# Kernel optimization log

Measured on AMD Instinct MI355X. Metric: run time of the kernel, lower is better.

## Reference

```python
import jax, jax.numpy as jnp
import numpy as np
import math

B, L, S, T = 16, 128, 128, 128
QDIM, FDIM, HID, ODIM = 512, 512, 512, 512

def setup_inputs() -> dict:
    key = jax.random.key(0)
    ks = jax.random.split(key, 9)
    sc = 0.02
    return {
        "query": jax.random.normal(ks[0], (B, L, QDIM), dtype=jnp.float32),
        "src": jax.random.normal(ks[1], (B, S, FDIM), dtype=jnp.float32),
        "trg": jax.random.normal(ks[2], (B, T, FDIM), dtype=jnp.float32),
        "Wq": jax.random.normal(ks[3], (QDIM, HID), dtype=jnp.float32) * sc,
        "bq": jnp.zeros((HID,), dtype=jnp.float32),
        "Ws": jax.random.normal(ks[4], (FDIM, HID), dtype=jnp.float32) * sc,
        "bs": jnp.zeros((HID,), dtype=jnp.float32),
        "Wo": jax.random.normal(ks[5], (FDIM * 2 + QDIM, ODIM), dtype=jnp.float32) * sc,
        "bo": jnp.zeros((ODIM,), dtype=jnp.float32),
    }

def reference(query, src, trg, Wq, bq, Ws, bs, Wo, bo):
    b, l, _ = query.shape
    s = src.shape[1]
    t = trg.shape[1]
    q = query @ Wq + bq            # [b,l,h]
    s_key = src @ Ws + bs          # [b,s,h]  (src_linear == trg_linear, shared weights)
    t_key = trg @ Ws + bs          # [b,t,h]
    # trilinear scores: [b,l,s,t]
    weight = jnp.einsum('blk,bsk,btk->blst', q, s_key, t_key) / math.sqrt(HID)
    weight = jax.nn.softmax(weight.reshape(b, l, s * t), axis=-1).reshape(b, l, s, t)
    s_ctx = jnp.einsum('blst,bsf->blf', weight, src)
    t_ctx = jnp.einsum('blst,btf->blf', weight, trg)
    x = jnp.concatenate((query, s_ctx, t_ctx), axis=-1)
    return x @ Wo + bo
```

## Files before the change

kernel.cpp:

```cpp
#include <hip/hip_runtime.h>
#include <hip/hip_bf16.h>

typedef __attribute__((ext_vector_type(8))) short short8;
typedef __attribute__((ext_vector_type(4))) short short4v;
typedef __attribute__((ext_vector_type(4))) float f32x4;
typedef __attribute__((ext_vector_type(8))) _Float16 half8;

#define DEVINL static __device__ __forceinline__

constexpr float SCORE_SCALE = 0.063758977414048896f;

typedef const __attribute__((address_space(1))) void gv_t;
typedef __attribute__((address_space(3))) void lv_t;
DEVINL void gload16(const void* g, void* l) {
  __builtin_amdgcn_global_load_lds((gv_t*)g, (lv_t*)l, 16, 0, 0);
}

#define SWZ_ADD(v, pat)                                                    \
  v += __int_as_float(__builtin_amdgcn_ds_swizzle(__float_as_int(v), pat))

template <int M, int N>
DEVINL void gemm16(const _Float16* A, const _Float16* B, int K, int lda, int ldb,
                   _Float16* ldsA, _Float16* ldsB, f32x4 acc[M / 32][N / 32])
{
  const int tid = threadIdx.x, lane = tid & 63;
  const int wr = (tid >> 7) & 1, wc = (tid >> 6) & 1;
  constexpr int MA = M / 32, NB = N / 32;
  int aoff[MA], boff[NB];
#pragma unroll
  for (int i = 0; i < MA; ++i) {
    const int ci = tid + i * 256, row = ci >> 3, c = ci & 7;
    aoff[i] = row * lda + ((c ^ (row & 7)) << 3);
  }
#pragma unroll
  for (int i = 0; i < NB; ++i) {
    const int ci = tid + i * 256, row = ci >> 3, c = ci & 7;
    boff[i] = row * ldb + ((c ^ (row & 7)) << 3);
  }
#define G16STAGE(cur, kk)                                                        \
  {                                                                              \
    _Pragma("unroll")                                                            \
    for (int i = 0; i < MA; ++i)                                                 \
      gload16(A + aoff[i] + (kk), ldsA + (cur) * (M * 64) + (tid + i * 256) * 8);\
    _Pragma("unroll")                                                            \
    for (int i = 0; i < NB; ++i)                                                 \
      gload16(B + boff[i] + (kk), ldsB + (cur) * (N * 64) + (tid + i * 256) * 8);\
  }
  G16STAGE(0, 0);
  __syncthreads();
  for (int kk = 0; kk < K; kk += 64) {
    const int cur = (kk >> 6) & 1;
    if (kk + 64 < K) G16STAGE(cur ^ 1, kk + 64);
    const _Float16* bA = ldsA + cur * (M * 64);
    const _Float16* bB = ldsB + cur * (N * 64);
#pragma unroll
    for (int s = 0; s < 2; ++s) {
      const int cg2 = s * 4 + (lane >> 4);
      half8 afr[MA], bfr[NB];
#pragma unroll
      for (int mi = 0; mi < MA; ++mi) {
        const int r = wr * (M / 2) + mi * 16 + (lane & 15);
        afr[mi] = *(const half8*)(bA + r * 64 + ((cg2 ^ (r & 7)) << 3));
      }
#pragma unroll
      for (int ni = 0; ni < NB; ++ni) {
        const int r = wc * (N / 2) + ni * 16 + (lane & 15);
        bfr[ni] = *(const half8*)(bB + r * 64 + ((cg2 ^ (r & 7)) << 3));
      }
#pragma unroll
      for (int mi = 0; mi < MA; ++mi)
#pragma unroll
        for (int ni = 0; ni < NB; ++ni)
          acc[mi][ni] = __builtin_amdgcn_mfma_f32_16x16x32_f16(afr[mi], bfr[ni], acc[mi][ni], 0, 0, 0);
    }
    __syncthreads();
  }
#undef G16STAGE
}

__global__ __launch_bounds__(256) void k_prep(
    const float* __restrict__ query, const float* __restrict__ src,
    const float* __restrict__ trg,
    const float* __restrict__ Wq, const float* __restrict__ Ws,
    const float* __restrict__ Wo,
    _Float16* __restrict__ x, _Float16* __restrict__ srch,
    _Float16* __restrict__ trgh,
    _Float16* __restrict__ WqT, _Float16* __restrict__ WsT,
    _Float16* __restrict__ WoT,
    _Float16* __restrict__ srcT, _Float16* __restrict__ trgT)
{
  __shared__ float t[32][33];
  const int id = blockIdx.x, tid = threadIdx.x;
  if (id < 1536) {
    const int z = id >> 9;
    const int idx8 = (((id & 511) << 8) + tid) * 8;
    const float* in = (z == 0) ? query : (z == 1) ? src : trg;
    float4 va = *(const float4*)(in + idx8);
    float4 vb = *(const float4*)(in + idx8 + 4);
    half8 h;
    h[0] = (_Float16)va.x; h[1] = (_Float16)va.y;
    h[2] = (_Float16)va.z; h[3] = (_Float16)va.w;
    h[4] = (_Float16)vb.x; h[5] = (_Float16)vb.y;
    h[6] = (_Float16)vb.z; h[7] = (_Float16)vb.w;
    if (z == 0) {
      const int row = idx8 >> 9, col = idx8 & 511;
      *(half8*)(x + (size_t)row * 1536 + col) = h;
    } else {
      _Float16* o = (z == 1) ? srch : trgh;
      *(half8*)(o + idx8) = h;
    }
    return;
  }
  const float* in; _Float16* out; int KK, NN, bx, by; size_t bo = 0;
  if (id < 1792)      { const int u = id - 1536; in = Wq;  out = WqT;  KK = 512;  NN = 512; bx = u & 15; by = u >> 4; }
  else if (id < 2048) { const int u = id - 1792; in = Ws;  out = WsT;  KK = 512;  NN = 512; bx = u & 15; by = u >> 4; }
  else if (id < 2816) { const int u = id - 2048; in = Wo;  out = WoT;  KK = 1536; NN = 512; bx = u & 15; by = u >> 4; }
  else if (id < 3840) { const int u = id - 2816; in = src; out = srcT; KK = 128;  NN = 512; bx = u & 15; by = (u >> 4) & 3; bo = (size_t)(u >> 6) * 65536; }
  else                { const int u = id - 3840; in = trg; out = trgT; KK = 128;  NN = 512; bx = u & 15; by = (u >> 4) & 3; bo = (size_t)(u >> 6) * 65536; }
  const int tx = tid & 31, ty = tid >> 5;
  const int k0 = by * 32, n0 = bx * 32;
#pragma unroll
  for (int i = 0; i < 4; ++i)
    t[ty + i * 8][tx] = in[bo + (size_t)(k0 + ty + i * 8) * NN + n0 + tx];
  __syncthreads();
#pragma unroll
  for (int i = 0; i < 4; ++i)
    out[bo + (size_t)(n0 + ty + i * 8) * KK + k0 + tx] = (_Float16)t[tx][ty + i * 8];
}

__global__ __launch_bounds__(256) void k_proj(
    const _Float16* __restrict__ xq, const _Float16* __restrict__ srch,
    const _Float16* __restrict__ trgh,
    const _Float16* __restrict__ WqT, const _Float16* __restrict__ WsT,
    const float* __restrict__ bq, const float* __restrict__ bs,
    _Float16* __restrict__ qh, _Float16* __restrict__ skh,
    _Float16* __restrict__ tkh)
{
  __shared__ __align__(16) _Float16 lds[24576];
  const int z = blockIdx.z;
  const _Float16* A = (z == 0) ? xq : (z == 1) ? srch : trgh;
  const int lda = (z == 0) ? 1536 : 512;
  const _Float16* BT = (z == 0) ? WqT : WsT;
  const float* bias = (z == 0) ? bq : bs;
  const int brow = blockIdx.y * 64, bcol = blockIdx.x * 128;

  f32x4 acc[2][4] = {};
  gemm16<64, 128>(A + (size_t)brow * lda, BT + (size_t)bcol * 512, 512, lda, 512,
                  lds, lds + 8192, acc);

  const int tid = threadIdx.x, lane = tid & 63;
  const int wr = (tid >> 7) & 1, wc = (tid >> 6) & 1;
  const int r0 = wr * 32 + ((lane >> 4) << 2);
  const int c0 = wc * 64 + (lane & 15);
#pragma unroll
  for (int mi = 0; mi < 2; ++mi)
#pragma unroll
    for (int ni = 0; ni < 4; ++ni) {
      const int col = bcol + c0 + ni * 16;
      const float bv = bias[col];
#pragma unroll
      for (int r = 0; r < 4; ++r) {
        const int row = brow + r0 + mi * 16 + r;
        const float v = acc[mi][ni][r] + bv;
        if (z == 0)      qh[(size_t)row * 512 + col] = (_Float16)(v * SCORE_SCALE);
        else if (z == 1) skh[(size_t)row * 512 + col] = (_Float16)v;
        else             tkh[(size_t)row * 512 + col] = (_Float16)v;
      }
    }
}

__global__ __launch_bounds__(512, 4) void k_score(
    const _Float16* __restrict__ qh, const _Float16* __restrict__ skh,
    const _Float16* __restrict__ tkh,
    _Float16* __restrict__ wct)
{
  __shared__ __align__(16) char pool[51200];
  _Float16* qlds = (_Float16*)(pool + 49152);
  float* wsp   = (float*)(pool);
  float* wtp   = (float*)(pool + 4096);
  float* wfin  = (float*)(pool + 8192);
  float* denom = (float*)(pool + 12288);

  const int raw = blockIdx.x;
  const int swz = (raw & 7) * 128 + (raw >> 3);
  const int b = swz >> 6, l0 = (swz & 63) * 2;

  const int tid = threadIdx.x, lane = tid & 63, wid = tid >> 6;
  const int l = wid >> 2, qs = (wid >> 1) & 1, qt = wid & 1;
  const int cg = lane >> 4;
  const int ln = lane & 15;
  const _Float16* skb = skh + (size_t)b * 65536;
  const _Float16* tkb = tkh + (size_t)b * 65536;

  int soff;
  {
    const int row = tid >> 2, c = tid & 3;
    soff = row * 512 + ((c ^ ((row >> 1) & 3)) << 3);
  }

  if (tid < 256) {
    const int li = tid >> 7, e = (tid & 127) * 4;
    *(short4v*)(qlds + li * 512 + e) =
        *(const short4v*)(qh + (size_t)(b * 128 + l0 + li) * 512 + e);
  }

  const int rbase_s = (qs * 64 + ln) * 64;
  const int rbase_t = (qt * 64 + ln) * 64;
  const int sw = (cg ^ ((ln >> 1) & 3)) << 4;

#define KSTAGE(dstbuf, kt)                                                  \
  {                                                                         \
    gload16(skb + soff + (kt) * 32, (dstbuf) + tid * 16);                   \
    gload16(tkb + soff + (kt) * 32, (dstbuf) + 8192 + tid * 16);            \
  }

  f32x4 acc[4][4] = {};
  char* bufA = pool;
  char* bufB = pool + 16384;
  char* bufC = pool + 32768;
  KSTAGE(bufA, 0);
  KSTAGE(bufB, 1);
  asm volatile("s_waitcnt vmcnt(0) lgkmcnt(0)" ::: "memory");
  __builtin_amdgcn_sched_barrier(0);
  __builtin_amdgcn_s_barrier();
  __builtin_amdgcn_sched_barrier(0);

  for (int it = 0; it < 16; ++it) {
    if (it < 14) KSTAGE(bufC, it + 2);
    half8 qv = *(const half8*)(qlds + l * 512 + it * 32 + cg * 8);
    half8 sfr[4], tfr[4];
#pragma unroll
    for (int mi = 0; mi < 4; ++mi)
      sfr[mi] = *(const half8*)(bufA + rbase_s + mi * 1024 + sw);
#pragma unroll
    for (int ni = 0; ni < 4; ++ni)
      tfr[ni] = *(const half8*)(bufA + 8192 + rbase_t + ni * 1024 + sw);
    __builtin_amdgcn_s_setprio(1);
#pragma unroll
    for (int mi = 0; mi < 4; ++mi) {
      half8 a = sfr[mi] * qv;
#pragma unroll
      for (int ni = 0; ni < 4; ++ni)
        acc[mi][ni] = __builtin_amdgcn_mfma_f32_16x16x32_f16(a, tfr[ni], acc[mi][ni], 0, 0, 0);
    }
    __builtin_amdgcn_s_setprio(0);
    if (it < 14) { asm volatile("s_waitcnt vmcnt(2)" ::: "memory"); }
    else         { asm volatile("s_waitcnt vmcnt(0)" ::: "memory"); }
    __builtin_amdgcn_sched_barrier(0);
    __builtin_amdgcn_s_barrier();
    __builtin_amdgcn_sched_barrier(0);
    char* t_ = bufA; bufA = bufB; bufB = bufC; bufC = t_;
  }
#undef KSTAGE

#pragma unroll
  for (int mi = 0; mi < 4; ++mi)
#pragma unroll
    for (int ni = 0; ni < 4; ++ni)
#pragma unroll
      for (int r = 0; r < 4; ++r)
        acc[mi][ni][r] = exp2f(acc[mi][ni][r]);

#pragma unroll
  for (int mi = 0; mi < 4; ++mi)
#pragma unroll
    for (int r = 0; r < 4; ++r) {
      float v = acc[mi][0][r] + acc[mi][1][r] + acc[mi][2][r] + acc[mi][3][r];
      SWZ_ADD(v, 0x041F);
      SWZ_ADD(v, 0x081F);
      SWZ_ADD(v, 0x101F);
      SWZ_ADD(v, 0x201F);
      if ((lane & 15) == 0)
        wsp[(l * 2 + qt) * 128 + qs * 64 + mi * 16 + (lane >> 4) * 4 + r] = v;
    }
#pragma unroll
  for (int ni = 0; ni < 4; ++ni) {
    float v = 0.f;
#pragma unroll
    for (int mi = 0; mi < 4; ++mi)
#pragma unroll
      for (int r = 0; r < 4; ++r) v += acc[mi][ni][r];
    SWZ_ADD(v, 0x401F);
    v += __shfl_xor(v, 32);
    if (lane < 16) wtp[(l * 2 + qs) * 128 + qt * 64 + ni * 16 + lane] = v;
  }
  __syncthreads();

  if (tid < 256) {
    const int li = tid >> 7, idx = tid & 127;
    wfin[(li * 2 + 0) * 128 + idx] =
        wsp[(li * 2 + 0) * 128 + idx] + wsp[(li * 2 + 1) * 128 + idx];
  } else {
    const int u = tid - 256, li = u >> 7, idx = u & 127;
    wfin[(li * 2 + 1) * 128 + idx] =
        wtp[(li * 2 + 0) * 128 + idx] + wtp[(li * 2 + 1) * 128 + idx];
  }
  __syncthreads();
  if (wid < 2) {
    float v = wfin[wid * 256 + lane] + wfin[wid * 256 + lane + 64];
#pragma unroll
    for (int off = 32; off >= 1; off >>= 1) v += __shfl_xor(v, off);
    if (lane == 0) denom[wid] = v;
  }
  __syncthreads();
  const float inv0 = 1.0f / denom[0], inv1 = 1.0f / denom[1];

  if (tid < 256) {
    const int li = tid >> 7, idx = tid & 127;
    const float inv = li ? inv1 : inv0;
    wct[((size_t)(b * 2 + 0) * 128 + l0 + li) * 128 + idx] =
        (_Float16)(wfin[li * 256 + idx] * inv);
  } else {
    const int u = tid - 256, li = u >> 7, idx = u & 127;
    const float inv = li ? inv1 : inv0;
    wct[((size_t)(b * 2 + 1) * 128 + l0 + li) * 128 + idx] =
        (_Float16)(wfin[li * 256 + 128 + idx] * inv);
  }
}

__global__ __launch_bounds__(256) void k_ctx(const _Float16* __restrict__ wct,
                                             const _Float16* __restrict__ srcT,
                                             const _Float16* __restrict__ trgT,
                                             _Float16* __restrict__ x)
{
  __shared__ __align__(16) _Float16 lds[24576];
  const int side = blockIdx.x, fcol = blockIdx.y >> 1, mrow = blockIdx.y & 1;
  const int b = blockIdx.z;
  const _Float16* A  = wct + (size_t)(b * 2 + side) * 16384 + mrow * 64 * 128;
  const _Float16* BT = (side ? trgT : srcT) + (size_t)b * 65536 + fcol * 16384;

  f32x4 acc[2][4] = {};
  gemm16<64, 128>(A, BT, 128, 128, 128, lds, lds + 8192, acc);

  const int tid = threadIdx.x, lane = tid & 63;
  const int wr = (tid >> 7) & 1, wc = (tid >> 6) & 1;
  const int r0 = wr * 32 + ((lane >> 4) << 2);
  const int c0 = wc * 64 + (lane & 15);
  const int xoff = 512 + side * 512 + fcol * 128;
#pragma unroll
  for (int mi = 0; mi < 2; ++mi)
#pragma unroll
    for (int ni = 0; ni < 4; ++ni) {
      const int col = c0 + ni * 16;
#pragma unroll
      for (int r = 0; r < 4; ++r) {
        const int row = mrow * 64 + r0 + mi * 16 + r;
        x[(size_t)(b * 128 + row) * 1536 + xoff + col] = (_Float16)acc[mi][ni][r];
      }
    }
}

__global__ __launch_bounds__(256) void k_out(const _Float16* __restrict__ x,
                                             const _Float16* __restrict__ WoT,
                                             const float* __restrict__ bo,
                                             float* __restrict__ out)
{
  __shared__ __align__(16) _Float16 lds[16384];
  const int brow = blockIdx.y * 64, bcol = blockIdx.x * 64;
  f32x4 acc[2][2] = {};
  gemm16<64, 64>(x + (size_t)brow * 1536, WoT + (size_t)bcol * 1536, 1536, 1536, 1536,
                 lds, lds + 8192, acc);
  const int tid = threadIdx.x, lane = tid & 63;
  const int wr = (tid >> 7) & 1, wc = (tid >> 6) & 1;
  const int r0 = wr * 32 + ((lane >> 4) << 2);
  const int c0 = wc * 32 + (lane & 15);
#pragma unroll
  for (int mi = 0; mi < 2; ++mi)
#pragma unroll
    for (int ni = 0; ni < 2; ++ni) {
      const int col = bcol + c0 + ni * 16;
      const float bv = bo[col];
#pragma unroll
      for (int r = 0; r < 4; ++r) {
        const int row = brow + r0 + mi * 16 + r;
        out[(size_t)row * 512 + col] = acc[mi][ni][r] + bv;
      }
    }
}

extern "C" void kernel_launch(void* const* d_in, const int* in_sizes, int n_in,
                              void* d_out, int out_size, void* d_ws, size_t ws_size,
                              hipStream_t stream)
{
  (void)in_sizes; (void)n_in; (void)out_size; (void)ws_size;
  const float* query = (const float*)d_in[0];
  const float* src   = (const float*)d_in[1];
  const float* trg   = (const float*)d_in[2];
  const float* Wq    = (const float*)d_in[3];
  const float* bq    = (const float*)d_in[4];
  const float* Ws    = (const float*)d_in[5];
  const float* bs    = (const float*)d_in[6];
  const float* Wo    = (const float*)d_in[7];
  const float* bo    = (const float*)d_in[8];
  float* out = (float*)d_out;

  char* w = (char*)d_ws;
  _Float16* x    = (_Float16*)(w);
  _Float16* qh   = (_Float16*)(w + (6u  << 20));
  _Float16* skh  = (_Float16*)(w + (8u  << 20));
  _Float16* tkh  = (_Float16*)(w + (10u << 20));
  _Float16* srch = (_Float16*)(w + (12u << 20));
  _Float16* trgh = (_Float16*)(w + (14u << 20));
  _Float16* WqT  = (_Float16*)(w + (16u << 20));
  _Float16* WsT  = (_Float16*)(w + (16u << 20) + 512 * 512 * 2);
  _Float16* WoT  = (_Float16*)(w + (17u << 20));
  _Float16* srcT = (_Float16*)(w + (19u << 20));
  _Float16* trgT = (_Float16*)(w + (21u << 20));
  _Float16* wct  = (_Float16*)(w + (23u << 20));

  k_prep<<<4864, 256, 0, stream>>>(query, src, trg, Wq, Ws, Wo,
                                   x, srch, trgh, WqT, WsT, WoT, srcT, trgT);
  k_proj<<<dim3(4, 32, 3), 256, 0, stream>>>(x, srch, trgh, WqT, WsT, bq, bs, qh, skh, tkh);
  k_score<<<1024, 512, 0, stream>>>(qh, skh, tkh, wct);
  k_ctx<<<dim3(2, 8, 16), 256, 0, stream>>>(wct, srcT, trgT, x);
  k_out<<<dim3(8, 32), 256, 0, stream>>>(x, WoT, bo, out);
}
```

Measured before the change: 79.52 us.

## Halve k_score block size, each wave computes both query rows

```diff
diff --git a/kernel.cpp b/kernel.cpp
--- a/kernel.cpp
+++ b/kernel.cpp
@@ -169,7 +169,7 @@
     }
 }
 
-__global__ __launch_bounds__(512, 4) void k_score(
+__global__ __launch_bounds__(256, 2) void k_score(
     const _Float16* __restrict__ qh, const _Float16* __restrict__ skh,
     const _Float16* __restrict__ tkh,
     _Float16* __restrict__ wct)
@@ -186,19 +186,21 @@
   const int b = swz >> 6, l0 = (swz & 63) * 2;
 
   const int tid = threadIdx.x, lane = tid & 63, wid = tid >> 6;
-  const int l = wid >> 2, qs = (wid >> 1) & 1, qt = wid & 1;
+  const int qs = wid >> 1, qt = wid & 1;
   const int cg = lane >> 4;
   const int ln = lane & 15;
   const _Float16* skb = skh + (size_t)b * 65536;
   const _Float16* tkb = tkh + (size_t)b * 65536;
 
-  int soff;
+  int soff[2];
+#pragma unroll
+  for (int j = 0; j < 2; ++j) {
+    const int ci = j * 256 + tid;
+    const int row = ci >> 2, c = ci & 3;
+    soff[j] = row * 512 + ((c ^ ((row >> 1) & 3)) << 3);
+  }
+
   {
-    const int row = tid >> 2, c = tid & 3;
-    soff = row * 512 + ((c ^ ((row >> 1) & 3)) << 3);
-  }
-
-  if (tid < 256) {
     const int li = tid >> 7, e = (tid & 127) * 4;
     *(short4v*)(qlds + li * 512 + e) =
         *(const short4v*)(qh + (size_t)(b * 128 + l0 + li) * 512 + e);
@@ -210,11 +212,14 @@
 
 #define KSTAGE(dstbuf, kt)                                                  \
   {                                                                         \
-    gload16(skb + soff + (kt) * 32, (dstbuf) + tid * 16);                   \
-    gload16(tkb + soff + (kt) * 32, (dstbuf) + 8192 + tid * 16);            \
-  }
-
-  f32x4 acc[4][4] = {};
+    _Pragma("unroll")                                                       \
+    for (int j = 0; j < 2; ++j) {                                           \
+      gload16(skb + soff[j] + (kt) * 32, (dstbuf) + (j * 256 + tid) * 16);  \
+      gload16(tkb + soff[j] + (kt) * 32, (dstbuf) + 8192 + (j * 256 + tid) * 16); \
+    }                                                                       \
+  }
+
+  f32x4 acc[2][4][4] = {};
   char* bufA = pool;
   char* bufB = pool + 16384;
   char* bufC = pool + 32768;
@@ -227,7 +232,8 @@
 
   for (int it = 0; it < 16; ++it) {
     if (it < 14) KSTAGE(bufC, it + 2);
-    half8 qv = *(const half8*)(qlds + l * 512 + it * 32 + cg * 8);
+    half8 qv0 = *(const half8*)(qlds + it * 32 + cg * 8);
+    half8 qv1 = *(const half8*)(qlds + 512 + it * 32 + cg * 8);
     half8 sfr[4], tfr[4];
 #pragma unroll
     for (int mi = 0; mi < 4; ++mi)
@@ -238,13 +244,16 @@
     __builtin_amdgcn_s_setprio(1);
 #pragma unroll
     for (int mi = 0; mi < 4; ++mi) {
-      half8 a = sfr[mi] * qv;
-#pragma unroll
-      for (int ni = 0; ni < 4; ++ni)
-        acc[mi][ni] = __builtin_amdgcn_mfma_f32_16x16x32_f16(a, tfr[ni], acc[mi][ni], 0, 0, 0);
+      half8 a0 = sfr[mi] * qv0;
+      half8 a1 = sfr[mi] * qv1;
+#pragma unroll
+      for (int ni = 0; ni < 4; ++ni) {
+        acc[0][mi][ni] = __builtin_amdgcn_mfma_f32_16x16x32_f16(a0, tfr[ni], acc[0][mi][ni], 0, 0, 0);
+        acc[1][mi][ni] = __builtin_amdgcn_mfma_f32_16x16x32_f16(a1, tfr[ni], acc[1][mi][ni], 0, 0, 0);
+      }
     }
     __builtin_amdgcn_s_setprio(0);
-    if (it < 14) { asm volatile("s_waitcnt vmcnt(2)" ::: "memory"); }
+    if (it < 14) { asm volatile("s_waitcnt vmcnt(4)" ::: "memory"); }
     else         { asm volatile("s_waitcnt vmcnt(0)" ::: "memory"); }
     __builtin_amdgcn_sched_barrier(0);
     __builtin_amdgcn_s_barrier();
@@ -254,46 +263,51 @@
 #undef KSTAGE
 
 #pragma unroll
-  for (int mi = 0; mi < 4; ++mi)
-#pragma unroll
-    for (int ni = 0; ni < 4; ++ni)
-#pragma unroll
-      for (int r = 0; r < 4; ++r)
-        acc[mi][ni][r] = exp2f(acc[mi][ni][r]);
-
-#pragma unroll
-  for (int mi = 0; mi < 4; ++mi)
-#pragma unroll
-    for (int r = 0; r < 4; ++r) {
-      float v = acc[mi][0][r] + acc[mi][1][r] + acc[mi][2][r] + acc[mi][3][r];
-      SWZ_ADD(v, 0x041F);
-      SWZ_ADD(v, 0x081F);
-      SWZ_ADD(v, 0x101F);
-      SWZ_ADD(v, 0x201F);
-      if ((lane & 15) == 0)
-        wsp[(l * 2 + qt) * 128 + qs * 64 + mi * 16 + (lane >> 4) * 4 + r] = v;
-    }
-#pragma unroll
-  for (int ni = 0; ni < 4; ++ni) {
-    float v = 0.f;
+  for (int li = 0; li < 2; ++li)
 #pragma unroll
     for (int mi = 0; mi < 4; ++mi)
 #pragma unroll
-      for (int r = 0; r < 4; ++r) v += acc[mi][ni][r];
-    SWZ_ADD(v, 0x401F);
-    v += __shfl_xor(v, 32);
-    if (lane < 16) wtp[(l * 2 + qs) * 128 + qt * 64 + ni * 16 + lane] = v;
-  }
+      for (int ni = 0; ni < 4; ++ni)
+#pragma unroll
+        for (int r = 0; r < 4; ++r)
+          acc[li][mi][ni][r] = exp2f(acc[li][mi][ni][r]);
+
+#pragma unroll
+  for (int li = 0; li < 2; ++li)
+#pragma unroll
+    for (int mi = 0; mi < 4; ++mi)
+#pragma unroll
+      for (int r = 0; r < 4; ++r) {
+        float v = acc[li][mi][0][r] + acc[li][mi][1][r] + acc[li][mi][2][r] + acc[li][mi][3][r];
+        SWZ_ADD(v, 0x041F);
+        SWZ_ADD(v, 0x081F);
+        SWZ_ADD(v, 0x101F);
+        SWZ_ADD(v, 0x201F);
+        if ((lane & 15) == 0)
+          wsp[(li * 2 + qt) * 128 + qs * 64 + mi * 16 + (lane >> 4) * 4 + r] = v;
+      }
+#pragma unroll
+  for (int li = 0; li < 2; ++li)
+#pragma unroll
+    for (int ni = 0; ni < 4; ++ni) {
+      float v = 0.f;
+#pragma unroll
+      for (int mi = 0; mi < 4; ++mi)
+#pragma unroll
+        for (int r = 0; r < 4; ++r) v += acc[li][mi][ni][r];
+      SWZ_ADD(v, 0x401F);
+      v += __shfl_xor(v, 32);
+      if (lane < 16) wtp[(li * 2 + qs) * 128 + qt * 64 + ni * 16 + lane] = v;
+    }
   __syncthreads();
 
-  if (tid < 256) {
-    const int li = tid >> 7, idx = tid & 127;
-    wfin[(li * 2 + 0) * 128 + idx] =
-        wsp[(li * 2 + 0) * 128 + idx] + wsp[(li * 2 + 1) * 128 + idx];
+  if (tid < 128) {
+    wfin[0 * 128 + tid] = wsp[0 * 128 + tid] + wsp[1 * 128 + tid];
+    wfin[2 * 128 + tid] = wsp[2 * 128 + tid] + wsp[3 * 128 + tid];
   } else {
-    const int u = tid - 256, li = u >> 7, idx = u & 127;
-    wfin[(li * 2 + 1) * 128 + idx] =
-        wtp[(li * 2 + 0) * 128 + idx] + wtp[(li * 2 + 1) * 128 + idx];
+    const int u = tid - 128;
+    wfin[1 * 128 + u] = wtp[0 * 128 + u] + wtp[1 * 128 + u];
+    wfin[3 * 128 + u] = wtp[2 * 128 + u] + wtp[3 * 128 + u];
   }
   __syncthreads();
   if (wid < 2) {
@@ -305,16 +319,13 @@
   __syncthreads();
   const float inv0 = 1.0f / denom[0], inv1 = 1.0f / denom[1];
 
-  if (tid < 256) {
-    const int li = tid >> 7, idx = tid & 127;
-    const float inv = li ? inv1 : inv0;
-    wct[((size_t)(b * 2 + 0) * 128 + l0 + li) * 128 + idx] =
-        (_Float16)(wfin[li * 256 + idx] * inv);
+  if (tid < 128) {
+    wct[((size_t)(b * 2 + 0) * 128 + l0 + 0) * 128 + tid] = (_Float16)(wfin[0 * 128 + tid] * inv0);
+    wct[((size_t)(b * 2 + 0) * 128 + l0 + 1) * 128 + tid] = (_Float16)(wfin[2 * 128 + tid] * inv1);
   } else {
-    const int u = tid - 256, li = u >> 7, idx = u & 127;
-    const float inv = li ? inv1 : inv0;
-    wct[((size_t)(b * 2 + 1) * 128 + l0 + li) * 128 + idx] =
-        (_Float16)(wfin[li * 256 + 128 + idx] * inv);
+    const int u = tid - 128;
+    wct[((size_t)(b * 2 + 1) * 128 + l0 + 0) * 128 + u] = (_Float16)(wfin[1 * 128 + u] * inv0);
+    wct[((size_t)(b * 2 + 1) * 128 + l0 + 1) * 128 + u] = (_Float16)(wfin[3 * 128 + u] * inv1);
   }
 }
 
@@ -411,7 +422,7 @@
   k_prep<<<4864, 256, 0, stream>>>(query, src, trg, Wq, Ws, Wo,
                                    x, srch, trgh, WqT, WsT, WoT, srcT, trgT);
   k_proj<<<dim3(4, 32, 3), 256, 0, stream>>>(x, srch, trgh, WqT, WsT, bq, bs, qh, skh, tkh);
-  k_score<<<1024, 512, 0, stream>>>(qh, skh, tkh, wct);
+  k_score<<<1024, 256, 0, stream>>>(qh, skh, tkh, wct);
   k_ctx<<<dim3(2, 8, 16), 256, 0, stream>>>(wct, srcT, trgT, x);
   k_out<<<dim3(8, 32), 256, 0, stream>>>(x, WoT, bo, out);
 }
```

Measured after the change: 84.91 us. +6.8%, slower.

## Reassociate context GEMMs by precomputing source/target projections through Wo

Applied to the files above, without the earlier changes.

```diff
diff --git a/kernel.cpp b/kernel.cpp
--- a/kernel.cpp
+++ b/kernel.cpp
@@ -83,11 +83,10 @@
     const float* __restrict__ trg,
     const float* __restrict__ Wq, const float* __restrict__ Ws,
     const float* __restrict__ Wo,
-    _Float16* __restrict__ x, _Float16* __restrict__ srch,
+    _Float16* __restrict__ qx, _Float16* __restrict__ srch,
     _Float16* __restrict__ trgh,
     _Float16* __restrict__ WqT, _Float16* __restrict__ WsT,
-    _Float16* __restrict__ WoT,
-    _Float16* __restrict__ srcT, _Float16* __restrict__ trgT)
+    _Float16* __restrict__ WoT)
 {
   __shared__ float t[32][33];
   const int id = blockIdx.x, tid = threadIdx.x;
@@ -102,71 +101,86 @@
     h[2] = (_Float16)va.z; h[3] = (_Float16)va.w;
     h[4] = (_Float16)vb.x; h[5] = (_Float16)vb.y;
     h[6] = (_Float16)vb.z; h[7] = (_Float16)vb.w;
-    if (z == 0) {
-      const int row = idx8 >> 9, col = idx8 & 511;
-      *(half8*)(x + (size_t)row * 1536 + col) = h;
-    } else {
-      _Float16* o = (z == 1) ? srch : trgh;
-      *(half8*)(o + idx8) = h;
-    }
+    _Float16* o = (z == 0) ? qx : (z == 1) ? srch : trgh;
+    *(half8*)(o + idx8) = h;
     return;
   }
-  const float* in; _Float16* out; int KK, NN, bx, by; size_t bo = 0;
-  if (id < 1792)      { const int u = id - 1536; in = Wq;  out = WqT;  KK = 512;  NN = 512; bx = u & 15; by = u >> 4; }
-  else if (id < 2048) { const int u = id - 1792; in = Ws;  out = WsT;  KK = 512;  NN = 512; bx = u & 15; by = u >> 4; }
-  else if (id < 2816) { const int u = id - 2048; in = Wo;  out = WoT;  KK = 1536; NN = 512; bx = u & 15; by = u >> 4; }
-  else if (id < 3840) { const int u = id - 2816; in = src; out = srcT; KK = 128;  NN = 512; bx = u & 15; by = (u >> 4) & 3; bo = (size_t)(u >> 6) * 65536; }
-  else                { const int u = id - 3840; in = trg; out = trgT; KK = 128;  NN = 512; bx = u & 15; by = (u >> 4) & 3; bo = (size_t)(u >> 6) * 65536; }
+  const float* in; _Float16* out; int KK, NN, bx, by;
+  if (id < 1792)      { const int u = id - 1536; in = Wq; out = WqT; KK = 512;  NN = 512; bx = u & 15; by = u >> 4; }
+  else if (id < 2048) { const int u = id - 1792; in = Ws; out = WsT; KK = 512;  NN = 512; bx = u & 15; by = u >> 4; }
+  else                { const int u = id - 2048; in = Wo; out = WoT; KK = 1536; NN = 512; bx = u & 15; by = u >> 4; }
   const int tx = tid & 31, ty = tid >> 5;
   const int k0 = by * 32, n0 = bx * 32;
 #pragma unroll
   for (int i = 0; i < 4; ++i)
-    t[ty + i * 8][tx] = in[bo + (size_t)(k0 + ty + i * 8) * NN + n0 + tx];
+    t[ty + i * 8][tx] = in[(size_t)(k0 + ty + i * 8) * NN + n0 + tx];
   __syncthreads();
 #pragma unroll
   for (int i = 0; i < 4; ++i)
-    out[bo + (size_t)(n0 + ty + i * 8) * KK + k0 + tx] = (_Float16)t[tx][ty + i * 8];
+    out[(size_t)(n0 + ty + i * 8) * KK + k0 + tx] = (_Float16)t[tx][ty + i * 8];
 }
 
 __global__ __launch_bounds__(256) void k_proj(
-    const _Float16* __restrict__ xq, const _Float16* __restrict__ srch,
+    const _Float16* __restrict__ qx, const _Float16* __restrict__ srch,
     const _Float16* __restrict__ trgh,
     const _Float16* __restrict__ WqT, const _Float16* __restrict__ WsT,
+    const _Float16* __restrict__ WoT,
     const float* __restrict__ bq, const float* __restrict__ bs,
     _Float16* __restrict__ qh, _Float16* __restrict__ skh,
-    _Float16* __restrict__ tkh)
+    _Float16* __restrict__ tkh,
+    _Float16* __restrict__ PsT, _Float16* __restrict__ PtT)
 {
   __shared__ __align__(16) _Float16 lds[24576];
-  const int z = blockIdx.z;
-  const _Float16* A = (z == 0) ? xq : (z == 1) ? srch : trgh;
-  const int lda = (z == 0) ? 1536 : 512;
-  const _Float16* BT = (z == 0) ? WqT : WsT;
-  const float* bias = (z == 0) ? bq : bs;
-  const int brow = blockIdx.y * 64, bcol = blockIdx.x * 128;
-
-  f32x4 acc[2][4] = {};
-  gemm16<64, 128>(A + (size_t)brow * lda, BT + (size_t)bcol * 512, 512, lda, 512,
-                  lds, lds + 8192, acc);
-
+  const int id = blockIdx.x;
   const int tid = threadIdx.x, lane = tid & 63;
   const int wr = (tid >> 7) & 1, wc = (tid >> 6) & 1;
   const int r0 = wr * 32 + ((lane >> 4) << 2);
   const int c0 = wc * 64 + (lane & 15);
-#pragma unroll
-  for (int mi = 0; mi < 2; ++mi)
-#pragma unroll
-    for (int ni = 0; ni < 4; ++ni) {
-      const int col = bcol + c0 + ni * 16;
-      const float bv = bias[col];
-#pragma unroll
-      for (int r = 0; r < 4; ++r) {
-        const int row = brow + r0 + mi * 16 + r;
-        const float v = acc[mi][ni][r] + bv;
-        if (z == 0)      qh[(size_t)row * 512 + col] = (_Float16)(v * SCORE_SCALE);
-        else if (z == 1) skh[(size_t)row * 512 + col] = (_Float16)v;
-        else             tkh[(size_t)row * 512 + col] = (_Float16)v;
+
+  f32x4 acc[2][4] = {};
+
+  if (id < 384) {
+    const int z = id >> 7, u = id & 127;
+    const int bcol = (u & 3) * 128, brow = (u >> 2) * 64;
+    const _Float16* A = (z == 0) ? qx : (z == 1) ? srch : trgh;
+    const _Float16* BT = (z == 0) ? WqT : WsT;
+    const float* bias = (z == 0) ? bq : bs;
+    gemm16<64, 128>(A + (size_t)brow * 512, BT + (size_t)bcol * 512,
+                    512, 512, 512, lds, lds + 8192, acc);
+#pragma unroll
+    for (int mi = 0; mi < 2; ++mi)
+#pragma unroll
+      for (int ni = 0; ni < 4; ++ni) {
+        const int col = bcol + c0 + ni * 16;
+        const float bv = bias[col];
+#pragma unroll
+        for (int r = 0; r < 4; ++r) {
+          const int row = brow + r0 + mi * 16 + r;
+          const float v = acc[mi][ni][r] + bv;
+          if (z == 0)      qh[(size_t)row * 512 + col] = (_Float16)(v * SCORE_SCALE);
+          else if (z == 1) skh[(size_t)row * 512 + col] = (_Float16)v;
+          else             tkh[(size_t)row * 512 + col] = (_Float16)v;
+        }
       }
-    }
+  } else {
+    const int side = (id - 384) >> 7, u = (id - 384) & 127;
+    const int b = u >> 3, brow = (u & 7) * 64;
+    const _Float16* A = WoT + (size_t)brow * 1536 + 512 + side * 512;
+    const _Float16* B = (side ? trgh : srch) + (size_t)b * 65536;
+    gemm16<64, 128>(A, B, 512, 1536, 512, lds, lds + 8192, acc);
+    _Float16* P = (side ? PtT : PsT) + (size_t)b * 65536;
+#pragma unroll
+    for (int mi = 0; mi < 2; ++mi)
+#pragma unroll
+      for (int ni = 0; ni < 4; ++ni) {
+        const int col = c0 + ni * 16;
+#pragma unroll
+        for (int r = 0; r < 4; ++r) {
+          const int row = brow + r0 + mi * 16 + r;
+          P[(size_t)row * 128 + col] = (_Float16)acc[mi][ni][r];
+        }
+      }
+  }
 }
 
 __global__ __launch_bounds__(512, 4) void k_score(
@@ -318,48 +332,26 @@
   }
 }
 
-__global__ __launch_bounds__(256) void k_ctx(const _Float16* __restrict__ wct,
-                                             const _Float16* __restrict__ srcT,
-                                             const _Float16* __restrict__ trgT,
-                                             _Float16* __restrict__ x)
-{
-  __shared__ __align__(16) _Float16 lds[24576];
-  const int side = blockIdx.x, fcol = blockIdx.y >> 1, mrow = blockIdx.y & 1;
-  const int b = blockIdx.z;
-  const _Float16* A  = wct + (size_t)(b * 2 + side) * 16384 + mrow * 64 * 128;
-  const _Float16* BT = (side ? trgT : srcT) + (size_t)b * 65536 + fcol * 16384;
-
-  f32x4 acc[2][4] = {};
-  gemm16<64, 128>(A, BT, 128, 128, 128, lds, lds + 8192, acc);
-
-  const int tid = threadIdx.x, lane = tid & 63;
-  const int wr = (tid >> 7) & 1, wc = (tid >> 6) & 1;
-  const int r0 = wr * 32 + ((lane >> 4) << 2);
-  const int c0 = wc * 64 + (lane & 15);
-  const int xoff = 512 + side * 512 + fcol * 128;
-#pragma unroll
-  for (int mi = 0; mi < 2; ++mi)
-#pragma unroll
-    for (int ni = 0; ni < 4; ++ni) {
-      const int col = c0 + ni * 16;
-#pragma unroll
-      for (int r = 0; r < 4; ++r) {
-        const int row = mrow * 64 + r0 + mi * 16 + r;
-        x[(size_t)(b * 128 + row) * 1536 + xoff + col] = (_Float16)acc[mi][ni][r];
-      }
-    }
-}
-
-__global__ __launch_bounds__(256) void k_out(const _Float16* __restrict__ x,
-                                             const _Float16* __restrict__ WoT,
-                                             const float* __restrict__ bo,
-                                             float* __restrict__ out)
+__global__ __launch_bounds__(256) void k_final(
+    const _Float16* __restrict__ qx, const _Float16* __restrict__ WoT,
+    const _Float16* __restrict__ wct,
+    const _Float16* __restrict__ PsT, const _Float16* __restrict__ PtT,
+    const float* __restrict__ bo, float* __restrict__ out)
 {
   __shared__ __align__(16) _Float16 lds[16384];
   const int brow = blockIdx.y * 64, bcol = blockIdx.x * 64;
+  const int b = blockIdx.y >> 1, half = blockIdx.y & 1;
+
   f32x4 acc[2][2] = {};
-  gemm16<64, 64>(x + (size_t)brow * 1536, WoT + (size_t)bcol * 1536, 1536, 1536, 1536,
-                 lds, lds + 8192, acc);
+  gemm16<64, 64>(qx + (size_t)brow * 512, WoT + (size_t)bcol * 1536,
+                 512, 512, 1536, lds, lds + 8192, acc);
+  gemm16<64, 64>(wct + (size_t)(b * 2 + 0) * 16384 + half * 8192,
+                 PsT + (size_t)b * 65536 + (size_t)bcol * 128,
+                 128, 128, 128, lds, lds + 8192, acc);
+  gemm16<64, 64>(wct + (size_t)(b * 2 + 1) * 16384 + half * 8192,
+                 PtT + (size_t)b * 65536 + (size_t)bcol * 128,
+                 128, 128, 128, lds, lds + 8192, acc);
+
   const int tid = threadIdx.x, lane = tid & 63;
   const int wr = (tid >> 7) & 1, wc = (tid >> 6) & 1;
   const int r0 = wr * 32 + ((lane >> 4) << 2);
@@ -395,23 +387,23 @@
   float* out = (float*)d_out;
 
   char* w = (char*)d_ws;
-  _Float16* x    = (_Float16*)(w);
-  _Float16* qh   = (_Float16*)(w + (6u  << 20));
-  _Float16* skh  = (_Float16*)(w + (8u  << 20));
-  _Float16* tkh  = (_Float16*)(w + (10u << 20));
-  _Float16* srch = (_Float16*)(w + (12u << 20));
-  _Float16* trgh = (_Float16*)(w + (14u << 20));
-  _Float16* WqT  = (_Float16*)(w + (16u << 20));
-  _Float16* WsT  = (_Float16*)(w + (16u << 20) + 512 * 512 * 2);
-  _Float16* WoT  = (_Float16*)(w + (17u << 20));
-  _Float16* srcT = (_Float16*)(w + (19u << 20));
-  _Float16* trgT = (_Float16*)(w + (21u << 20));
-  _Float16* wct  = (_Float16*)(w + (23u << 20));
-
-  k_prep<<<4864, 256, 0, stream>>>(query, src, trg, Wq, Ws, Wo,
-                                   x, srch, trgh, WqT, WsT, WoT, srcT, trgT);
-  k_proj<<<dim3(4, 32, 3), 256, 0, stream>>>(x, srch, trgh, WqT, WsT, bq, bs, qh, skh, tkh);
+  _Float16* qx   = (_Float16*)(w);
+  _Float16* qh   = (_Float16*)(w + (2u  << 20));
+  _Float16* skh  = (_Float16*)(w + (4u  << 20));
+  _Float16* tkh  = (_Float16*)(w + (6u  << 20));
+  _Float16* srch = (_Float16*)(w + (8u  << 20));
+  _Float16* trgh = (_Float16*)(w + (10u << 20));
+  _Float16* WqT  = (_Float16*)(w + (12u << 20));
+  _Float16* WsT  = (_Float16*)(w + (13u << 20));
+  _Float16* WoT  = (_Float16*)(w + (14u << 20));
+  _Float16* wct  = (_Float16*)(w + (16u << 20));
+  _Float16* PsT  = (_Float16*)(w + (17u << 20));
+  _Float16* PtT  = (_Float16*)(w + (19u << 20));
+
+  k_prep<<<2816, 256, 0, stream>>>(query, src, trg, Wq, Ws, Wo,
+                                   qx, srch, trgh, WqT, WsT, WoT);
+  k_proj<<<640, 256, 0, stream>>>(qx, srch, trgh, WqT, WsT, WoT, bq, bs,
+                                  qh, skh, tkh, PsT, PtT);
   k_score<<<1024, 512, 0, stream>>>(qh, skh, tkh, wct);
-  k_ctx<<<dim3(2, 8, 16), 256, 0, stream>>>(wct, srcT, trgT, x);
-  k_out<<<dim3(8, 32), 256, 0, stream>>>(x, WoT, bo, out);
-}
+  k_final<<<dim3(8, 32), 256, 0, stream>>>(qx, WoT, wct, PsT, PtT, bo, out);
+}
```

New measurement: 70.47 us. -11.4%, faster.
